# Kernel tuning notes

Measured on AMD Instinct MI355X. Metric: run time of the kernel, lower is better.

The kernel has to match this reference:

```python
import jax, jax.numpy as jnp
import numpy as np

C = 1.0          # Poincare ball curvature
TEMP = 0.1       # softmax temperature
EPS = 1e-15
TANH_CLIP = 1.0 - 1e-5


def setup_inputs() -> dict:
    key = jax.random.key(0)
    ks = jax.random.split(key, 9)
    B, Din, H, D, P = 2048, 1024, 4096, 128, 1000
    inp = {
        "x": jax.random.normal(ks[0], (B, Din), dtype=jnp.float32),
        "W1": jax.random.normal(ks[1], (Din, H), dtype=jnp.float32) / np.sqrt(Din),
        "b1": jnp.zeros((H,), dtype=jnp.float32),
        "W2": jax.random.normal(ks[2], (H, H), dtype=jnp.float32) / np.sqrt(H),
        "b2": jnp.zeros((H,), dtype=jnp.float32),
        "W3": jax.random.normal(ks[3], (H, D), dtype=jnp.float32) / np.sqrt(H),
        "b3": jnp.zeros((D,), dtype=jnp.float32),
        # prototypes: points inside the unit ball (norm ~ 0.2)
        "prototypes": jax.random.normal(ks[4], (P, D), dtype=jnp.float32) * 0.02,
    }
    return inp


def _expmap0(u):
    sqc = np.sqrt(C)
    n = jnp.maximum(jnp.linalg.norm(u, axis=-1, keepdims=True), EPS)
    return jnp.tanh(sqc * n) * u / (sqc * n)


def _logmap0(y):
    sqc = np.sqrt(C)
    n = jnp.maximum(jnp.linalg.norm(y, axis=-1, keepdims=True), EPS)
    arg = jnp.clip(sqc * n, 0.0, TANH_CLIP)
    return jnp.arctanh(arg) * y / (sqc * n)


def _pairwise_dist(proto, xh):
    # dist(x=proto[P,D], y=xh[B,D]) = (2/sqrt(c)) * artanh(sqrt(c)*||(-x) (+) y||)
    # Mobius add norm computed from Gram products only (no [B,P,D] intermediate).
    # a = -proto, b = xh
    a2 = jnp.sum(proto * proto, axis=-1)          # [P]  ||a||^2
    b2 = jnp.sum(xh * xh, axis=-1)                # [B]  ||b||^2
    ab = -jnp.einsum('bd,pd->bp', xh, proto)      # [B,P] <a,b>
    a2_ = a2[None, :]
    b2_ = b2[:, None]
    alpha = 1.0 + 2.0 * C * ab + C * b2_
    beta = 1.0 - C * a2_
    gamma = 1.0 + 2.0 * C * ab + (C * C) * a2_ * b2_
    m2 = (alpha * alpha * a2_ + 2.0 * alpha * beta * ab + beta * beta * b2_) / (gamma * gamma)
    mnorm = jnp.sqrt(jnp.maximum(m2, 0.0))
    sqc = np.sqrt(C)
    arg = jnp.clip(sqc * mnorm, 0.0, TANH_CLIP)
    return (2.0 / sqc) * jnp.arctanh(arg)         # [B,P]


def reference(x, W1, b1, W2, b2, W3, b3, prototypes):
    h = jax.nn.gelu(x @ W1 + b1, approximate=False)
    h = jax.nn.gelu(h @ W2 + b2, approximate=False)
    u = h @ W3 + b3                               # [B,D]
    x_hyp = _expmap0(u)
    dists = _pairwise_dist(prototypes, x_hyp)     # [B,P]
    logits = -dists / TEMP
    pred = jnp.argmax(logits, axis=1)             # [B]
    pred_protos = jax.lax.stop_gradient(prototypes[pred])  # detach, as in torch
    feedback = _logmap0(pred_protos)              # [B,D]
    return logits, feedback
```

## Files before the change

### kernel.cpp

```cpp
#include <hip/hip_runtime.h>
#include <math.h>

#define B_SZ 2048
#define DIN  1024
#define H_SZ 4096
#define D_SZ 128
#define P_SZ 1000
#define PPAD 1024

typedef __attribute__((ext_vector_type(8))) short bf16x8;
typedef __attribute__((ext_vector_type(4))) float f32x4;

__device__ __forceinline__ float gelu_exact(float v) {
    return 0.5f * v * (1.0f + erff(v * 0.70710678118654752f));
}

__device__ __forceinline__ short f2bf(float f) {
    unsigned u = __float_as_uint(f);
    u = (u + 0x7fffu + ((u >> 16) & 1u)) >> 16;
    return (short)u;
}

__device__ __forceinline__ void gload_lds16(const void* g, void* l) {
    __builtin_amdgcn_global_load_lds(
        (__attribute__((address_space(1))) void*)(uintptr_t)g,
        (__attribute__((address_space(3))) void*)(uintptr_t)l,
        16, 0, 0);
}

__device__ __forceinline__ void trans_tile(
    const float* __restrict__ W, short* __restrict__ WT, int K, int N,
    int bx, int by, int tid, float (*t)[65])
{
    const int n0 = bx * 64, k0 = by * 64;
    #pragma unroll
    for (int i = 0; i < 4; ++i) {
        const int idx = i * 256 + tid;
        const int r  = idx >> 4;
        const int c4 = (idx & 15) * 4;
        const float4 v = *reinterpret_cast<const float4*>(&W[(size_t)(k0 + r) * N + n0 + c4]);
        t[r][c4 + 0] = v.x; t[r][c4 + 1] = v.y; t[r][c4 + 2] = v.z; t[r][c4 + 3] = v.w;
    }
    __syncthreads();
    #pragma unroll
    for (int i = 0; i < 2; ++i) {
        const int idx = i * 256 + tid;
        const int n  = idx >> 3;
        const int kc = (idx & 7) * 8;
        bf16x8 o;
        #pragma unroll
        for (int q = 0; q < 8; ++q) o[q] = f2bf(t[kc + q][n]);
        *reinterpret_cast<bf16x8*>(&WT[(size_t)(n0 + n) * K + k0 + kc]) = o;
    }
}

__global__ __launch_bounds__(256) void prep_kernel(
    const float* __restrict__ x,     short* __restrict__ xb,
    const float* __restrict__ W1,    short* __restrict__ w1t,
    const float* __restrict__ W2,    short* __restrict__ w2t,
    const float* __restrict__ W3,    short* __restrict__ w3t,
    const float* __restrict__ proto, short* __restrict__ protob,
    float* __restrict__ a2gp)
{
    __shared__ float t[64][65];
    __shared__ float part[4];
    const int b = blockIdx.x;
    const int tid = threadIdx.x;

    if (b < 2048) {
        const int i = b * 1024 + tid * 4;
        const float4 v = *reinterpret_cast<const float4*>(&x[i]);
        short4 o;
        o.x = f2bf(v.x); o.y = f2bf(v.y); o.z = f2bf(v.z); o.w = f2bf(v.w);
        *reinterpret_cast<short4*>(&xb[i]) = o;
    } else if (b < 3072) {
        const int tt = b - 2048;
        trans_tile(W1, w1t, DIN, H_SZ, tt & 63, tt >> 6, tid, t);
    } else if (b < 7168) {
        const int tt = b - 3072;
        trans_tile(W2, w2t, H_SZ, H_SZ, tt & 63, tt >> 6, tid, t);
    } else if (b < 7296) {
        const int tt = b - 7168;
        trans_tile(W3, w3t, H_SZ, D_SZ, tt & 1, tt >> 1, tid, t);
    } else {
        const int h = tid >> 7;
        const int d = tid & 127;
        const int p = (b - 7296) * 2 + h;
        const float y = (p < P_SZ) ? proto[(size_t)p * D_SZ + d] : 0.f;
        protob[(size_t)p * D_SZ + d] = f2bf(y);
        float s = y * y;
        #pragma unroll
        for (int off = 32; off; off >>= 1) s += __shfl_down(s, off);
        if ((tid & 63) == 0) part[tid >> 6] = s;
        __syncthreads();
        if (d == 0) a2gp[p] = part[h * 2] + part[h * 2 + 1];
    }
}

template<int EPI>
__global__ __launch_bounds__(512) void gemm_big(
    const short* __restrict__ A, const short* __restrict__ BT,
    const float* __restrict__ bias, void* __restrict__ Cout,
    int M, int N, int K)
{
    extern __shared__ __align__(16) char smem[];

    const int tid  = threadIdx.x;
    const int lane = tid & 63;
    const int wid  = tid >> 6;
    const int row0 = blockIdx.y * 256;
    const int col0 = blockIdx.x * 128;
    const int wm = (wid >> 1) * 64;
    const int wn = (wid & 1) * 64;
    const int lr = lane & 15, kq = lane >> 4;

    const int kpb    = K / gridDim.z;
    const int kstart = blockIdx.z * kpb;
    const int NT = kpb >> 6;

    f32x4 acc[4][4];
    #pragma unroll
    for (int i = 0; i < 4; ++i)
        #pragma unroll
        for (int j = 0; j < 4; ++j) acc[i][j] = (f32x4){0.f, 0.f, 0.f, 0.f};

    const int srow = lane >> 3;
    const int kch  = (lane & 7) ^ srow;
    const short* Ag = A  + (size_t)(row0 + wid * 32 + srow) * K + kstart + kch * 8;
    const short* Bg = BT + (size_t)(col0 + wid * 16 + srow) * K + kstart + kch * 8;

    auto stage = [&](int t) {
        const int buf = t % 3;
        char* sA = smem + buf * 49152;
        char* sB = sA + 32768;
        const int k0 = t << 6;
        #pragma unroll
        for (int ii = 0; ii < 4; ++ii)
            gload_lds16(Ag + (size_t)ii * 8 * K + k0, sA + (wid * 4 + ii) * 1024);
        #pragma unroll
        for (int ii = 0; ii < 2; ++ii)
            gload_lds16(Bg + (size_t)ii * 8 * K + k0, sB + (wid * 2 + ii) * 1024);
    };

    auto read_frags = [&](const char* sA, const char* sB, int ks,
                          bf16x8* af, bf16x8* bfv) {
        #pragma unroll
        for (int i = 0; i < 4; ++i)
            af[i] = *reinterpret_cast<const bf16x8*>(
                sA + (wm + i * 16 + lr) * 128 + (((ks * 4 + kq) ^ (lr & 7)) * 16));
        #pragma unroll
        for (int j = 0; j < 4; ++j)
            bfv[j] = *reinterpret_cast<const bf16x8*>(
                sB + (wn + j * 16 + lr) * 128 + (((ks * 4 + kq) ^ (lr & 7)) * 16));
    };

    stage(0);
    stage(1);
    asm volatile("s_waitcnt vmcnt(6)" ::: "memory");
    __builtin_amdgcn_s_barrier();
    asm volatile("" ::: "memory");

    for (int t = 0; t < NT; ++t) {
        const bool more = (t + 2) < NT;
        const char* sA = smem + (t % 3) * 49152;
        const char* sB = sA + 32768;
        bf16x8 af[4], bfv[4];

        read_frags(sA, sB, 0, af, bfv);
        if (more) stage(t + 2);
        asm volatile("" ::: "memory");
        __builtin_amdgcn_s_barrier();
        asm volatile("s_waitcnt lgkmcnt(0)" ::: "memory");
        __builtin_amdgcn_sched_barrier(0);
        __builtin_amdgcn_s_setprio(1);
        #pragma unroll
        for (int i = 0; i < 4; ++i)
            #pragma unroll
            for (int j = 0; j < 4; ++j)
                acc[i][j] = __builtin_amdgcn_mfma_f32_16x16x32_bf16(
                    af[i], bfv[j], acc[i][j], 0, 0, 0);
        __builtin_amdgcn_s_setprio(0);
        asm volatile("" ::: "memory");
        __builtin_amdgcn_s_barrier();

        read_frags(sA, sB, 1, af, bfv);
        if (more) asm volatile("s_waitcnt vmcnt(6)" ::: "memory");
        else      asm volatile("s_waitcnt vmcnt(0)" ::: "memory");
        __builtin_amdgcn_s_barrier();
        asm volatile("s_waitcnt lgkmcnt(0)" ::: "memory");
        __builtin_amdgcn_sched_barrier(0);
        __builtin_amdgcn_s_setprio(1);
        #pragma unroll
        for (int i = 0; i < 4; ++i)
            #pragma unroll
            for (int j = 0; j < 4; ++j)
                acc[i][j] = __builtin_amdgcn_mfma_f32_16x16x32_bf16(
                    af[i], bfv[j], acc[i][j], 0, 0, 0);
        __builtin_amdgcn_s_setprio(0);
        asm volatile("" ::: "memory");
        __builtin_amdgcn_s_barrier();
    }

    #pragma unroll
    for (int j = 0; j < 4; ++j) {
        const int col = col0 + wn + j * 16 + lr;
        const float bv = (EPI == 0) ? bias[col] : 0.f;
        #pragma unroll
        for (int i = 0; i < 4; ++i) {
            #pragma unroll
            for (int q = 0; q < 4; ++q) {
                const int row = row0 + wm + i * 16 + kq * 4 + q;
                if (EPI == 0) {
                    float v = gelu_exact(acc[i][j][q] + bv);
                    ((short*)Cout)[(size_t)row * N + col] = f2bf(v);
                } else {
                    ((float*)Cout)[((size_t)blockIdx.z * M + row) * N + col] = acc[i][j][q];
                }
            }
        }
    }
}

__global__ __launch_bounds__(128) void expmap_kernel(
    const float* __restrict__ up, const float* __restrict__ b3,
    short* __restrict__ xhb, float* __restrict__ rowb2)
{
    const int b = blockIdx.x;
    const int d = threadIdx.x;
    float u = b3[d];
    #pragma unroll
    for (int z = 0; z < 16; ++z)
        u += up[((size_t)z * B_SZ + b) * D_SZ + d];

    float s = u * u;
    #pragma unroll
    for (int off = 32; off; off >>= 1) s += __shfl_down(s, off);
    __shared__ float part[2];
    if ((d & 63) == 0) part[d >> 6] = s;
    __syncthreads();
    const float n2 = part[0] + part[1];

    const float n = fmaxf(sqrtf(n2), 1e-15f);
    const float t = tanhf(n);
    xhb[(size_t)b * D_SZ + d] = f2bf(u * (t / n));
    if (d == 0) rowb2[b] = t * t;
}

__global__ __launch_bounds__(256) void dist_mfma(
    const short* __restrict__ xhb, const short* __restrict__ protob,
    const float* __restrict__ rowb2, const float* __restrict__ a2gp,
    float* __restrict__ logits)
{
    __shared__ __align__(16) char xs[128 * 256];
    __shared__ __align__(16) char ps[64 * 256];

    const int tid  = threadIdx.x;
    const int lane = tid & 63, wid = tid >> 6;
    const int pt = blockIdx.x * 64;
    const int bt = blockIdx.y * 128;
    const int wm = (wid >> 1) * 64;
    const int wn = (wid & 1) * 32;
    const int lr = lane & 15, kq = lane >> 4;

    const int rl = lane >> 4, c = lane & 15;
    #pragma unroll
    for (int i = 0; i < 8; ++i) {
        const int row = wid * 32 + i * 4 + rl;
        const int lc  = (c & 8) | ((c & 7) ^ (row & 7));
        gload_lds16(xhb + (size_t)(bt + row) * D_SZ + lc * 8,
                    xs + (wid * 8 + i) * 1024);
    }
    #pragma unroll
    for (int i = 0; i < 4; ++i) {
        const int row = wid * 16 + i * 4 + rl;
        const int lc  = (c & 8) | ((c & 7) ^ (row & 7));
        gload_lds16(protob + (size_t)(pt + row) * D_SZ + lc * 8,
                    ps + (wid * 4 + i) * 1024);
    }
    __syncthreads();

    f32x4 acc[4][2];
    #pragma unroll
    for (int i = 0; i < 4; ++i)
        #pragma unroll
        for (int j = 0; j < 2; ++j) acc[i][j] = (f32x4){0.f, 0.f, 0.f, 0.f};

    #pragma unroll
    for (int ks = 0; ks < 4; ++ks) {
        const int kslot = ks * 4 + kq;
        bf16x8 af[4], bfv[2];
        #pragma unroll
        for (int i = 0; i < 4; ++i) {
            const int row = wm + i * 16 + lr;
            const int ph = (kslot & 8) | ((kslot & 7) ^ (row & 7));
            af[i] = *reinterpret_cast<const bf16x8*>(xs + row * 256 + ph * 16);
        }
        #pragma unroll
        for (int j = 0; j < 2; ++j) {
            const int row = wn + j * 16 + lr;
            const int ph = (kslot & 8) | ((kslot & 7) ^ (row & 7));
            bfv[j] = *reinterpret_cast<const bf16x8*>(ps + row * 256 + ph * 16);
        }
        #pragma unroll
        for (int i = 0; i < 4; ++i)
            #pragma unroll
            for (int j = 0; j < 2; ++j)
                acc[i][j] = __builtin_amdgcn_mfma_f32_16x16x32_bf16(
                    af[i], bfv[j], acc[i][j], 0, 0, 0);
    }

    #pragma unroll
    for (int j = 0; j < 2; ++j) {
        const int p = pt + wn + j * 16 + lr;
        if (p < P_SZ) {
            const float a2 = a2gp[p];
            #pragma unroll
            for (int i = 0; i < 4; ++i) {
                #pragma unroll
                for (int q = 0; q < 4; ++q) {
                    const int b = bt + wm + i * 16 + kq * 4 + q;
                    const float b2 = rowb2[b];
                    const float ab = -acc[i][j][q];
                    const float alpha = 1.f + 2.f * ab + b2;
                    const float beta  = 1.f - a2;
                    const float gamma = 1.f + 2.f * ab + a2 * b2;
                    const float num = alpha * alpha * a2 + 2.f * alpha * beta * ab + beta * beta * b2;
                    const float m2 = num / (gamma * gamma);
                    const float mn = sqrtf(fmaxf(m2, 0.f));
                    const float arg = fminf(mn, 0.99999f);
                    const float dist = logf((1.f + arg) / (1.f - arg));
                    logits[(size_t)b * P_SZ + p] = -10.f * dist;
                }
            }
        }
    }
}

__global__ __launch_bounds__(256) void head_kernel(
    const float* __restrict__ logits, const float* __restrict__ proto,
    float* __restrict__ fb)
{
    const int b = blockIdx.x;
    const int tid = threadIdx.x;

    float best = -INFINITY; int bi = 0;
    for (int p = tid; p < P_SZ; p += 256) {
        const float v = logits[(size_t)b * P_SZ + p];
        if (v > best) { best = v; bi = p; }
    }
    __shared__ float bv[256];
    __shared__ int   bidx[256];
    bv[tid] = best; bidx[tid] = bi;
    __syncthreads();
    for (int s = 128; s; s >>= 1) {
        if (tid < s) {
            const float ov = bv[tid + s]; const int oi = bidx[tid + s];
            if (ov > bv[tid] || (ov == bv[tid] && oi < bidx[tid])) { bv[tid] = ov; bidx[tid] = oi; }
        }
        __syncthreads();
    }
    const int pred = bidx[0];
    __syncthreads();

    float y = 0.f;
    if (tid < 128) y = proto[(size_t)pred * D_SZ + tid];
    bv[tid] = y * y;
    __syncthreads();
    for (int s = 128; s; s >>= 1) {
        if (tid < s) bv[tid] += bv[tid + s];
        __syncthreads();
    }
    const float n2 = bv[0];
    if (tid < 128) {
        const float n = fmaxf(sqrtf(n2), 1e-15f);
        const float arg = fminf(n, 0.99999f);
        const float at = 0.5f * logf((1.f + arg) / (1.f - arg));
        fb[(size_t)b * D_SZ + tid] = at * (y / n);
    }
}

extern "C" void kernel_launch(void* const* d_in, const int* in_sizes, int n_in,
                              void* d_out, int out_size, void* d_ws, size_t ws_size,
                              hipStream_t stream)
{
    const float* x     = (const float*)d_in[0];
    const float* W1    = (const float*)d_in[1];
    const float* b1    = (const float*)d_in[2];
    const float* W2    = (const float*)d_in[3];
    const float* b2v   = (const float*)d_in[4];
    const float* W3    = (const float*)d_in[5];
    const float* b3    = (const float*)d_in[6];
    const float* proto = (const float*)d_in[7];

    float* logits = (float*)d_out;
    float* fb     = logits + (size_t)B_SZ * P_SZ;

    short* xb     = (short*)d_ws;
    short* w1t    = xb    + (size_t)B_SZ * DIN;
    short* w2t    = w1t   + (size_t)H_SZ * DIN;
    short* w3t    = w2t   + (size_t)H_SZ * H_SZ;
    short* h1     = w3t   + (size_t)D_SZ * H_SZ;
    short* h2     = h1    + (size_t)B_SZ * H_SZ;
    short* xhb    = h2    + (size_t)B_SZ * H_SZ;
    short* protob = xhb   + (size_t)B_SZ * D_SZ;
    float* rowb2  = (float*)(protob + (size_t)PPAD * D_SZ);
    float* a2gp   = rowb2 + B_SZ;
    float* up     = (float*)h1;

    static_cast<void>(hipFuncSetAttribute(
        reinterpret_cast<const void*>(&gemm_big<0>),
        hipFuncAttributeMaxDynamicSharedMemorySize, 3 * 49152));
    static_cast<void>(hipFuncSetAttribute(
        reinterpret_cast<const void*>(&gemm_big<1>),
        hipFuncAttributeMaxDynamicSharedMemorySize, 3 * 49152));

    prep_kernel<<<7808, 256, 0, stream>>>(x, xb, W1, w1t, W2, w2t, W3, w3t,
                                          proto, protob, a2gp);

    gemm_big<0><<<dim3(H_SZ / 128, B_SZ / 256), 512, 3 * 49152, stream>>>(
        xb, w1t, b1, h1, B_SZ, H_SZ, DIN);
    gemm_big<0><<<dim3(H_SZ / 128, B_SZ / 256), 512, 3 * 49152, stream>>>(
        h1, w2t, b2v, h2, B_SZ, H_SZ, H_SZ);
    gemm_big<1><<<dim3(1, B_SZ / 256, 16), 512, 3 * 49152, stream>>>(
        h2, w3t, nullptr, up, B_SZ, D_SZ, H_SZ);

    expmap_kernel<<<B_SZ, 128, 0, stream>>>(up, b3, xhb, rowb2);
    dist_mfma<<<dim3(PPAD / 64, B_SZ / 128), 256, 0, stream>>>(
        xhb, protob, rowb2, a2gp, logits);
    head_kernel<<<B_SZ, 256, 0, stream>>>(logits, proto, fb);
}
```

Before: 278.6 us.

## Restructure GEMM main loop to one barrier per k-tile; add 128x128 tile kernel for layer 1

The big GEMM main loop is rewritten so the next stage's global-to-LDS loads are issued at the top of each k-tile. Both k-substeps are then computed back to back, and a single combined vmcnt/lgkmcnt wait and barrier comes at the end, replacing four barriers per tile. A new 256-thread GEMM kernel with 128x128 tiles, a 32-wide k-step and static LDS (triple-buffered, k-chunk-major layout) is added and used for the first layer. That layer has K=1024, so the smaller tile doubles the block count and improves CU occupancy. Risks: the new LDS layout has no XOR swizzle and may cause bank conflicts, and fewer barriers change how loads overlap with MFMA.

```diff
diff --git a/kernel.cpp b/kernel.cpp
--- a/kernel.cpp
+++ b/kernel.cpp
@@ -142,18 +142,6 @@
             gload_lds16(Bg + (size_t)ii * 8 * K + k0, sB + (wid * 2 + ii) * 1024);
     };
 
-    auto read_frags = [&](const char* sA, const char* sB, int ks,
-                          bf16x8* af, bf16x8* bfv) {
-        #pragma unroll
-        for (int i = 0; i < 4; ++i)
-            af[i] = *reinterpret_cast<const bf16x8*>(
-                sA + (wm + i * 16 + lr) * 128 + (((ks * 4 + kq) ^ (lr & 7)) * 16));
-        #pragma unroll
-        for (int j = 0; j < 4; ++j)
-            bfv[j] = *reinterpret_cast<const bf16x8*>(
-                sB + (wn + j * 16 + lr) * 128 + (((ks * 4 + kq) ^ (lr & 7)) * 16));
-    };
-
     stage(0);
     stage(1);
     asm volatile("s_waitcnt vmcnt(6)" ::: "memory");
@@ -162,43 +150,41 @@
 
     for (int t = 0; t < NT; ++t) {
         const bool more = (t + 2) < NT;
+        if (more) stage(t + 2);
+
         const char* sA = smem + (t % 3) * 49152;
         const char* sB = sA + 32768;
-        bf16x8 af[4], bfv[4];
-
-        read_frags(sA, sB, 0, af, bfv);
-        if (more) stage(t + 2);
+
+        #pragma unroll
+        for (int ks = 0; ks < 2; ++ks) {
+            bf16x8 af[4], bfv[4];
+            #pragma unroll
+            for (int i = 0; i < 4; ++i) {
+                const int row = wm + i * 16 + lr;
+                af[i] = *reinterpret_cast<const bf16x8*>(
+                    sA + row * 128 + (((ks * 4 + kq) ^ (lr & 7)) * 16));
+            }
+            #pragma unroll
+            for (int j = 0; j < 4; ++j) {
+                const int row = wn + j * 16 + lr;
+                bfv[j] = *reinterpret_cast<const bf16x8*>(
+                    sB + row * 128 + (((ks * 4 + kq) ^ (lr & 7)) * 16));
+            }
+            __builtin_amdgcn_s_setprio(1);
+            #pragma unroll
+            for (int i = 0; i < 4; ++i)
+                #pragma unroll
+                for (int j = 0; j < 4; ++j)
+                    acc[i][j] = __builtin_amdgcn_mfma_f32_16x16x32_bf16(
+                        af[i], bfv[j], acc[i][j], 0, 0, 0);
+            __builtin_amdgcn_s_setprio(0);
+        }
+
         asm volatile("" ::: "memory");
+        if (more) asm volatile("s_waitcnt vmcnt(6) lgkmcnt(0)" ::: "memory");
+        else      asm volatile("s_waitcnt vmcnt(0) lgkmcnt(0)" ::: "memory");
         __builtin_amdgcn_s_barrier();
-        asm volatile("s_waitcnt lgkmcnt(0)" ::: "memory");
-        __builtin_amdgcn_sched_barrier(0);
-        __builtin_amdgcn_s_setprio(1);
-        #pragma unroll
-        for (int i = 0; i < 4; ++i)
-            #pragma unroll
-            for (int j = 0; j < 4; ++j)
-                acc[i][j] = __builtin_amdgcn_mfma_f32_16x16x32_bf16(
-                    af[i], bfv[j], acc[i][j], 0, 0, 0);
-        __builtin_amdgcn_s_setprio(0);
         asm volatile("" ::: "memory");
-        __builtin_amdgcn_s_barrier();
-
-        read_frags(sA, sB, 1, af, bfv);
-        if (more) asm volatile("s_waitcnt vmcnt(6)" ::: "memory");
-        else      asm volatile("s_waitcnt vmcnt(0)" ::: "memory");
-        __builtin_amdgcn_s_barrier();
-        asm volatile("s_waitcnt lgkmcnt(0)" ::: "memory");
-        __builtin_amdgcn_sched_barrier(0);
-        __builtin_amdgcn_s_setprio(1);
-        #pragma unroll
-        for (int i = 0; i < 4; ++i)
-            #pragma unroll
-            for (int j = 0; j < 4; ++j)
-                acc[i][j] = __builtin_amdgcn_mfma_f32_16x16x32_bf16(
-                    af[i], bfv[j], acc[i][j], 0, 0, 0);
-        __builtin_amdgcn_s_setprio(0);
-        asm volatile("" ::: "memory");
-        __builtin_amdgcn_s_barrier();
     }
 
     #pragma unroll
@@ -216,6 +202,95 @@
                 } else {
                     ((float*)Cout)[((size_t)blockIdx.z * M + row) * N + col] = acc[i][j][q];
                 }
+            }
+        }
+    }
+}
+
+__global__ __launch_bounds__(256) void gemm_m128(
+    const short* __restrict__ A, const short* __restrict__ BT,
+    const float* __restrict__ bias, short* __restrict__ Cout,
+    int M, int N, int K)
+{
+    __shared__ __align__(16) short sA[3][4][128][8];
+    __shared__ __align__(16) short sB[3][4][128][8];
+
+    const int tid  = threadIdx.x;
+    const int lane = tid & 63;
+    const int wid  = tid >> 6;
+    const int row0 = blockIdx.y * 128;
+    const int col0 = blockIdx.x * 128;
+    const int wm = (wid >> 1) * 64;
+    const int wn = (wid & 1) * 64;
+    const int lr = lane & 15, kq = lane >> 4;
+
+    const int NT = K >> 5;
+
+    f32x4 acc[4][4];
+    #pragma unroll
+    for (int i = 0; i < 4; ++i)
+        #pragma unroll
+        for (int j = 0; j < 4; ++j) acc[i][j] = (f32x4){0.f, 0.f, 0.f, 0.f};
+
+    const short* Ag = A  + (size_t)(row0 + lane) * K + wid * 8;
+    const short* Bg = BT + (size_t)(col0 + lane) * K + wid * 8;
+
+    auto stage = [&](int t) {
+        const int buf = t % 3;
+        const int k0 = t << 5;
+        #pragma unroll
+        for (int ii = 0; ii < 2; ++ii) {
+            gload_lds16(Ag + (size_t)(ii * 64) * K + k0, &sA[buf][wid][ii * 64][0]);
+            gload_lds16(Bg + (size_t)(ii * 64) * K + k0, &sB[buf][wid][ii * 64][0]);
+        }
+    };
+
+    stage(0);
+    stage(1);
+    asm volatile("s_waitcnt vmcnt(4)" ::: "memory");
+    __builtin_amdgcn_s_barrier();
+    asm volatile("" ::: "memory");
+
+    for (int t = 0; t < NT; ++t) {
+        const bool more = (t + 2) < NT;
+        if (more) stage(t + 2);
+        const int buf = t % 3;
+
+        bf16x8 af[4], bfv[4];
+        #pragma unroll
+        for (int i = 0; i < 4; ++i)
+            af[i] = *reinterpret_cast<const bf16x8*>(&sA[buf][kq][wm + i * 16 + lr][0]);
+        #pragma unroll
+        for (int j = 0; j < 4; ++j)
+            bfv[j] = *reinterpret_cast<const bf16x8*>(&sB[buf][kq][wn + j * 16 + lr][0]);
+
+        __builtin_amdgcn_s_setprio(1);
+        #pragma unroll
+        for (int i = 0; i < 4; ++i)
+            #pragma unroll
+            for (int j = 0; j < 4; ++j)
+                acc[i][j] = __builtin_amdgcn_mfma_f32_16x16x32_bf16(
+                    af[i], bfv[j], acc[i][j], 0, 0, 0);
+        __builtin_amdgcn_s_setprio(0);
+
+        asm volatile("" ::: "memory");
+        if (more) asm volatile("s_waitcnt vmcnt(4) lgkmcnt(0)" ::: "memory");
+        else      asm volatile("s_waitcnt vmcnt(0) lgkmcnt(0)" ::: "memory");
+        __builtin_amdgcn_s_barrier();
+        asm volatile("" ::: "memory");
+    }
+
+    #pragma unroll
+    for (int j = 0; j < 4; ++j) {
+        const int col = col0 + wn + j * 16 + lr;
+        const float bv = bias[col];
+        #pragma unroll
+        for (int i = 0; i < 4; ++i) {
+            #pragma unroll
+            for (int q = 0; q < 4; ++q) {
+                const int row = row0 + wm + i * 16 + kq * 4 + q;
+                float v = gelu_exact(acc[i][j][q] + bv);
+                Cout[(size_t)row * N + col] = f2bf(v);
             }
         }
     }
@@ -417,7 +492,7 @@
     prep_kernel<<<7808, 256, 0, stream>>>(x, xb, W1, w1t, W2, w2t, W3, w3t,
                                           proto, protob, a2gp);
 
-    gemm_big<0><<<dim3(H_SZ / 128, B_SZ / 256), 512, 3 * 49152, stream>>>(
+    gemm_m128<<<dim3(H_SZ / 128, B_SZ / 128), 256, 0, stream>>>(
         xb, w1t, b1, h1, B_SZ, H_SZ, DIN);
     gemm_big<0><<<dim3(H_SZ / 128, B_SZ / 256), 512, 3 * 49152, stream>>>(
         h1, w2t, b2v, h2, B_SZ, H_SZ, H_SZ);
```

Result: no change. 280.3 us (+0.6%).
